# Kernel tuning notes

Hardware: AMD Instinct MI355X
Metric: run time of the kernel (lower is better)

## Reference

```python
import jax, jax.numpy as jnp
import numpy as np
import math

N_HEAD = 16

def _rope(x):
    # x: [B, H, T, D], D even; interleaved-pair rotation as in the torch code
    B, H, T, D = x.shape
    theta = 10000.0 ** (-2.0 * jnp.arange(D // 2, dtype=x.dtype) / D)  # [D/2]
    pos = jnp.arange(T, dtype=x.dtype)[:, None]                        # [T,1]
    ang = pos * theta[None, :]                                          # [T, D/2]
    sin, cos = jnp.sin(ang), jnp.cos(ang)
    x1, x2 = x[..., ::2], x[..., 1::2]
    x1r = x1 * cos - x2 * sin
    x2r = x1 * sin + x2 * cos
    # re-interleave
    out = jnp.stack([x1r, x2r], axis=-1).reshape(B, H, T, D)
    return out

def setup_inputs() -> dict:
    key = jax.random.key(0)
    ks = jax.random.split(key, 3)
    B, T, C = 4, 2048, 1024
    x = jax.random.normal(ks[0], (B, T, C), dtype=jnp.float32)
    W_qkv = jax.random.normal(ks[1], (C, 3 * C), dtype=jnp.float32) * (1.0 / math.sqrt(C))
    b_qkv = jnp.zeros((3 * C,), dtype=jnp.float32)
    W_proj = jax.random.normal(ks[2], (C, C), dtype=jnp.float32) * (1.0 / math.sqrt(C))
    b_proj = jnp.zeros((C,), dtype=jnp.float32)
    return {"x": x, "W_qkv": W_qkv, "b_qkv": b_qkv, "W_proj": W_proj, "b_proj": b_proj}

def reference(x, W_qkv, b_qkv, W_proj, b_proj):
    B, T, C = x.shape
    H = N_HEAD
    D = C // H
    qkv = x @ W_qkv + b_qkv                      # [B,T,3C]
    q, k, v = jnp.split(qkv, 3, axis=-1)
    def to_heads(t):
        return t.reshape(B, T, H, D).transpose(0, 2, 1, 3)  # [B,H,T,D]
    q, k, v = to_heads(q), to_heads(k), to_heads(v)
    q = _rope(q)
    k = _rope(k)
    att = jnp.einsum('bhqd,bhkd->bhqk', q, k) * (1.0 / math.sqrt(D))
    mask = jnp.tril(jnp.ones((T, T), dtype=bool))
    att = jnp.where(mask[None, None, :, :], att, -jnp.inf)
    att = jax.nn.softmax(att, axis=-1)
    y = jnp.einsum('bhqk,bhkd->bhqd', att, v)    # [B,H,T,D]
    y = y.transpose(0, 2, 1, 3).reshape(B, T, C)
    return y @ W_proj + b_proj
```

## Files before the change

### kernel.cpp

```cpp
#include <hip/hip_runtime.h>
#include <cstddef>

#define B_DIM 4
#define T_DIM 2048
#define C_DIM 1024
#define H_DIM 16
#define D_DIM 64
#define C3_DIM 3072

typedef __attribute__((ext_vector_type(8))) _Float16 f16x8;
typedef __attribute__((ext_vector_type(4))) _Float16 f16x4;
typedef __attribute__((ext_vector_type(4))) float f32x4;

typedef const __attribute__((address_space(1))) unsigned int* gptr_t;
typedef __attribute__((address_space(3))) unsigned int* lptr_t;

#define QSCALE 0.180336850073f
#define NTHETA 0.41524101186f

__global__ __launch_bounds__(256) void prep(
    const float* __restrict__ x, _Float16* __restrict__ xh,
    const float* __restrict__ Wq, _Float16* __restrict__ Wqt,
    const float* __restrict__ Wp, _Float16* __restrict__ Wpt)
{
    __shared__ float tile[64][65];
    const int z = blockIdx.x, tid = threadIdx.x;

    if (z < 8192) {
        size_t i = (size_t)z * 1024 + tid * 4;
        float4 v = *(const float4*)&x[i];
        f16x4 o = { (_Float16)v.x, (_Float16)v.y, (_Float16)v.z, (_Float16)v.w };
        *(f16x4*)&xh[i] = o;
        return;
    }

    const float* W;
    _Float16* Wt;
    int N, idx;
    if (z < 8960) { W = Wq; Wt = Wqt; N = C3_DIM; idx = z - 8192; }
    else          { W = Wp; Wt = Wpt; N = C_DIM;  idx = z - 8960; }
    const int K = C_DIM;
    const int nblk = N / 64;
    const int n0 = (idx % nblk) * 64, k0 = (idx / nblk) * 64;

    const int tx = tid & 15, ty = tid >> 4;
#pragma unroll
    for (int it = 0; it < 4; ++it) {
        int r = it * 16 + ty;
        *(float4*)&tile[r][tx * 4] =
            *(const float4*)&W[(size_t)(k0 + r) * N + n0 + tx * 4];
    }
    __syncthreads();
    int c = tid >> 2, t0 = (tid & 3) * 16;
    __align__(16) _Float16 tmp[16];
#pragma unroll
    for (int j = 0; j < 16; ++j) tmp[j] = (_Float16)tile[t0 + j][c];
    _Float16* o = Wt + (size_t)(n0 + c) * K + k0 + t0;
    *(f16x8*)o = *(f16x8*)&tmp[0];
    *(f16x8*)(o + 8) = *(f16x8*)&tmp[8];
}

#define ISSUE_SLICE(BUF, S, KT)                                               \
    do {                                                                      \
        const _Float16* agk = ag + (KT) * 64 + (S) * 32;                      \
        const _Float16* bgk = bg + (KT) * 64 + (S) * 32;                      \
        __builtin_amdgcn_global_load_lds((gptr_t)(const void*)(agk),          \
            (lptr_t)(void*)&Af[BUF][S][w * 2 + 0][0][0], 16, 0, 0);           \
        __builtin_amdgcn_global_load_lds((gptr_t)(const void*)(agk + 16 * K), \
            (lptr_t)(void*)&Af[BUF][S][w * 2 + 1][0][0], 16, 0, 0);           \
        __builtin_amdgcn_global_load_lds((gptr_t)(const void*)(bgk),          \
            (lptr_t)(void*)&Bf[BUF][S][w][0][0], 16, 0, 0);                   \
    } while (0)

#define COMPUTE_SLICE(BUF, S, SWAPPED)                                        \
    do {                                                                      \
        f16x8 av[4], bv[4];                                                   \
        _Pragma("unroll")                                                     \
        for (int i = 0; i < 4; ++i) {                                         \
            av[i] = *(const f16x8*)&Af[BUF][S][wm * 4 + i][lane][0];          \
            bv[i] = *(const f16x8*)&Bf[BUF][S][wn * 4 + i][lane][0];          \
        }                                                                     \
        __builtin_amdgcn_s_setprio(1);                                        \
        _Pragma("unroll")                                                     \
        for (int i = 0; i < 4; ++i)                                           \
            _Pragma("unroll")                                                 \
            for (int j = 0; j < 4; ++j)                                       \
                acc[i][j] = (SWAPPED)                                         \
                    ? __builtin_amdgcn_mfma_f32_16x16x32_f16(                 \
                          bv[j], av[i], acc[i][j], 0, 0, 0)                   \
                    : __builtin_amdgcn_mfma_f32_16x16x32_f16(                 \
                          av[i], bv[j], acc[i][j], 0, 0, 0);                  \
        __builtin_amdgcn_s_setprio(0);                                        \
    } while (0)

#define KLOOP(SWAPPED)                                                        \
    do {                                                                      \
        const int NT = K / 64;                                                \
        ISSUE_SLICE(0, 0, 0);                                                 \
        ISSUE_SLICE(0, 1, 0);                                                 \
        for (int t = 0; t < NT - 1; ++t) {                                    \
            const int cb = t & 1, nb = cb ^ 1;                                \
            ISSUE_SLICE(nb, 0, t + 1);                                        \
            asm volatile("s_waitcnt vmcnt(6)" ::: "memory");                  \
            __builtin_amdgcn_s_barrier();                                     \
            COMPUTE_SLICE(cb, 0, SWAPPED);                                    \
            ISSUE_SLICE(nb, 1, t + 1);                                        \
            asm volatile("s_waitcnt vmcnt(6)" ::: "memory");                  \
            __builtin_amdgcn_s_barrier();                                     \
            COMPUTE_SLICE(cb, 1, SWAPPED);                                    \
        }                                                                     \
        {                                                                     \
            const int cb = (NT - 1) & 1;                                      \
            asm volatile("s_waitcnt vmcnt(3)" ::: "memory");                  \
            __builtin_amdgcn_s_barrier();                                     \
            COMPUTE_SLICE(cb, 0, SWAPPED);                                    \
            asm volatile("s_waitcnt vmcnt(0)" ::: "memory");                  \
            __builtin_amdgcn_s_barrier();                                     \
            COMPUTE_SLICE(cb, 1, SWAPPED);                                    \
        }                                                                     \
    } while (0)

__global__ __launch_bounds__(512, 2) void gemm_qkv(
    const _Float16* __restrict__ A, const _Float16* __restrict__ Bt,
    const float* __restrict__ bias,
    _Float16* __restrict__ Qb, _Float16* __restrict__ Kb, _Float16* __restrict__ Vt)
{
    __shared__ __align__(16) _Float16 Af[2][2][16][64][8];
    __shared__ __align__(16) _Float16 Bf[2][2][8][64][8];
    const int tid = threadIdx.x;
    const int lane = tid & 63, w = tid >> 6;
    const int lm = lane & 15, lq = lane >> 4;
    const int wm = w >> 1, wn = w & 1;
    const int m0 = blockIdx.y * 256, n0 = blockIdx.x * 128;
    const int K = C_DIM;

    const _Float16* ag = A + (size_t)(m0 + w * 32 + lm) * K + lq * 8;
    const _Float16* bg = Bt + (size_t)(n0 + w * 16 + lm) * K + lq * 8;

    f32x4 acc[4][4];
#pragma unroll
    for (int i = 0; i < 4; ++i)
#pragma unroll
        for (int j = 0; j < 4; ++j) acc[i][j] = (f32x4){0.f, 0.f, 0.f, 0.f};

    const bool is_v = (n0 >= 2 * C_DIM);

    if (!is_v) {
        KLOOP(true);

        const bool is_q = (n0 < C_DIM);
        const float scale = is_q ? QSCALE : 1.0f;
        _Float16* dstbase = is_q ? Qb : Kb;
#pragma unroll
        for (int j = 0; j < 4; ++j) {
            int col = n0 + wn * 64 + j * 16 + lq * 4;
            int d0 = col & 63;
            int h = (col & (C_DIM - 1)) >> 6;
            float4 b4 = *(const float4*)&bias[col];
            float th0 = exp2f(-NTHETA * (float)(d0 >> 1));
            float th1 = exp2f(-NTHETA * (float)((d0 >> 1) + 1));
#pragma unroll
            for (int i = 0; i < 4; ++i) {
                int tg = m0 + wm * 64 + i * 16 + lm;
                int bb = tg >> 11, tl = tg & (T_DIM - 1);
                float v0 = acc[i][j][0] + b4.x;
                float v1 = acc[i][j][1] + b4.y;
                float v2 = acc[i][j][2] + b4.z;
                float v3 = acc[i][j][3] + b4.w;
                float s0, c0, s1, c1;
                __sincosf((float)tl * th0, &s0, &c0);
                __sincosf((float)tl * th1, &s1, &c1);
                f16x4 o = { (_Float16)((v0 * c0 - v1 * s0) * scale),
                            (_Float16)((v0 * s0 + v1 * c0) * scale),
                            (_Float16)((v2 * c1 - v3 * s1) * scale),
                            (_Float16)((v2 * s1 + v3 * c1) * scale) };
                *(f16x4*)&dstbase[((size_t)(bb * 16 + h) * T_DIM + tl) * 64 + d0] = o;
            }
        }
    } else {
        KLOOP(false);

#pragma unroll
        for (int i = 0; i < 4; ++i) {
            int t4 = m0 + wm * 64 + i * 16 + lq * 4;
            int bb = t4 >> 11, tl = t4 & (T_DIM - 1);
#pragma unroll
            for (int j = 0; j < 4; ++j) {
                int col = n0 + wn * 64 + j * 16 + lm;
                int dfull = col - 2 * C_DIM;
                int h = dfull >> 6, d = dfull & 63;
                float bc = bias[col];
                f16x4 o = { (_Float16)(acc[i][j][0] + bc),
                            (_Float16)(acc[i][j][1] + bc),
                            (_Float16)(acc[i][j][2] + bc),
                            (_Float16)(acc[i][j][3] + bc) };
                *(f16x4*)&Vt[((size_t)(bb * 16 + h) * 64 + d) * T_DIM + tl] = o;
            }
        }
    }
}

template <bool OUT_HALF>
__global__ __launch_bounds__(512, 2) void gemm_bt(
    const _Float16* __restrict__ A, const _Float16* __restrict__ Bt,
    const float* __restrict__ bias, void* __restrict__ Cout,
    int M, int N, int K)
{
    __shared__ __align__(16) _Float16 Af[2][2][16][64][8];
    __shared__ __align__(16) _Float16 Bf[2][2][8][64][8];
    const int tid = threadIdx.x;
    const int lane = tid & 63, w = tid >> 6;
    const int lm = lane & 15, lq = lane >> 4;
    const int wm = w >> 1, wn = w & 1;
    const int m0 = blockIdx.y * 256, n0 = blockIdx.x * 128;

    const _Float16* ag = A + (size_t)(m0 + w * 32 + lm) * K + lq * 8;
    const _Float16* bg = Bt + (size_t)(n0 + w * 16 + lm) * K + lq * 8;

    f32x4 acc[4][4];
#pragma unroll
    for (int i = 0; i < 4; ++i)
#pragma unroll
        for (int j = 0; j < 4; ++j) acc[i][j] = (f32x4){0.f, 0.f, 0.f, 0.f};

    KLOOP(true);

#pragma unroll
    for (int i = 0; i < 4; ++i) {
        size_t row = (size_t)(m0 + wm * 64 + i * 16 + lm);
#pragma unroll
        for (int j = 0; j < 4; ++j) {
            int col = n0 + wn * 64 + j * 16 + lq * 4;
            float4 b4 = *(const float4*)&bias[col];
            float v0 = acc[i][j][0] + b4.x;
            float v1 = acc[i][j][1] + b4.y;
            float v2 = acc[i][j][2] + b4.z;
            float v3 = acc[i][j][3] + b4.w;
            if (OUT_HALF) {
                f16x4 o = { (_Float16)v0, (_Float16)v1, (_Float16)v2, (_Float16)v3 };
                *(f16x4*)&((_Float16*)Cout)[row * N + col] = o;
            } else {
                float4 o = make_float4(v0, v1, v2, v3);
                *(float4*)&((float*)Cout)[row * N + col] = o;
            }
        }
    }
}

__global__ __launch_bounds__(256) void attn_mfma(
    const _Float16* __restrict__ Qb, const _Float16* __restrict__ Kb,
    const _Float16* __restrict__ Vt, _Float16* __restrict__ yb)
{
    __shared__ __align__(16) _Float16 Kf[8][64][8];
    __shared__ __align__(16) _Float16 Vf[8][64][8];
    __shared__ __align__(16) _Float16 Pb[4][16][72];

    const int tid = threadIdx.x;
    const int bh = blockIdx.x;
    const int qt = 31 - blockIdx.y;
    const int b = bh >> 4, h = bh & 15;
    const int lane = tid & 63, w = tid >> 6;
    const int m = lane & 15, qq = lane >> 4;

    const _Float16* qrow = Qb +
        ((size_t)bh * T_DIM + qt * 64 + w * 16 + m) * D_DIM + qq * 8;
    f16x8 qreg[2];
    qreg[0] = *(const f16x8*)qrow;
    qreg[1] = *(const f16x8*)(qrow + 32);

    float m_i = -1e30f, l_i = 0.f;
    f32x4 acc[4];
#pragma unroll
    for (int db = 0; db < 4; ++db) acc[db] = (f32x4){0.f, 0.f, 0.f, 0.f};

    const _Float16* kg0 = Kb + (size_t)bh * T_DIM * D_DIM +
                          (size_t)(w * 16 + m) * D_DIM + qq * 8;
    const _Float16* vg0 = Vt + (size_t)bh * D_DIM * T_DIM +
                          (size_t)(w * 16 + m) * T_DIM + qq * 8;

    f16x8 kr0 = *(const f16x8*)(kg0);
    f16x8 kr1 = *(const f16x8*)(kg0 + 32);
    f16x8 vr0 = *(const f16x8*)(vg0);
    f16x8 vr1 = *(const f16x8*)(vg0 + 32);

    for (int kt = 0; kt <= qt; ++kt) {
        __syncthreads();
        *(f16x8*)&Kf[w * 2 + 0][lane][0] = kr0;
        *(f16x8*)&Kf[w * 2 + 1][lane][0] = kr1;
        *(f16x8*)&Vf[w * 2 + 0][lane][0] = vr0;
        *(f16x8*)&Vf[w * 2 + 1][lane][0] = vr1;
        __syncthreads();

        int ktn = (kt < qt) ? kt + 1 : kt;
        kr0 = *(const f16x8*)(kg0 + (size_t)ktn * 64 * D_DIM);
        kr1 = *(const f16x8*)(kg0 + (size_t)ktn * 64 * D_DIM + 32);
        vr0 = *(const f16x8*)(vg0 + ktn * 64);
        vr1 = *(const f16x8*)(vg0 + ktn * 64 + 32);

        f32x4 sv[4];
#pragma unroll
        for (int nb = 0; nb < 4; ++nb) {
            f32x4 s = (f32x4){0.f, 0.f, 0.f, 0.f};
            s = __builtin_amdgcn_mfma_f32_16x16x32_f16(
                *(const f16x8*)&Kf[nb * 2 + 0][lane][0], qreg[0], s, 0, 0, 0);
            s = __builtin_amdgcn_mfma_f32_16x16x32_f16(
                *(const f16x8*)&Kf[nb * 2 + 1][lane][0], qreg[1], s, 0, 0, 0);
            sv[nb] = s;
        }

        if (kt == qt) {
            int qlocal = w * 16 + m;
#pragma unroll
            for (int nb = 0; nb < 4; ++nb) {
                int tb = nb * 16 + qq * 4;
#pragma unroll
                for (int r = 0; r < 4; ++r)
                    if (tb + r > qlocal) sv[nb][r] = -1e30f;
            }
        }

        float mt0 = fmaxf(fmaxf(sv[0][0], sv[0][1]), fmaxf(sv[0][2], sv[0][3]));
        float mt1 = fmaxf(fmaxf(sv[1][0], sv[1][1]), fmaxf(sv[1][2], sv[1][3]));
        float mt2 = fmaxf(fmaxf(sv[2][0], sv[2][1]), fmaxf(sv[2][2], sv[2][3]));
        float mt3 = fmaxf(fmaxf(sv[3][0], sv[3][1]), fmaxf(sv[3][2], sv[3][3]));
        float mt = fmaxf(fmaxf(mt0, mt1), fmaxf(mt2, mt3));
        mt = fmaxf(mt, __shfl_xor(mt, 16));
        mt = fmaxf(mt, __shfl_xor(mt, 32));
        float mnew = fmaxf(m_i, mt);
        float alpha = exp2f(m_i - mnew);
        float ll = 0.f;
#pragma unroll
        for (int nb = 0; nb < 4; ++nb) {
            float p0 = exp2f(sv[nb][0] - mnew);
            float p1 = exp2f(sv[nb][1] - mnew);
            float p2 = exp2f(sv[nb][2] - mnew);
            float p3 = exp2f(sv[nb][3] - mnew);
            sv[nb][0] = p0; sv[nb][1] = p1; sv[nb][2] = p2; sv[nb][3] = p3;
            ll += (p0 + p1) + (p2 + p3);
        }
        ll += __shfl_xor(ll, 16);
        ll += __shfl_xor(ll, 32);
        l_i = l_i * alpha + ll;
        m_i = mnew;
#pragma unroll
        for (int db = 0; db < 4; ++db) {
            acc[db][0] *= alpha; acc[db][1] *= alpha;
            acc[db][2] *= alpha; acc[db][3] *= alpha;
        }

#pragma unroll
        for (int nb = 0; nb < 4; ++nb) {
            f16x4 pv = { (_Float16)sv[nb][0], (_Float16)sv[nb][1],
                         (_Float16)sv[nb][2], (_Float16)sv[nb][3] };
            *(f16x4*)&Pb[w][m][nb * 16 + qq * 4] = pv;
        }

        f16x8 pf0 = *(const f16x8*)&Pb[w][m][0 * 32 + qq * 8];
        f16x8 pf1 = *(const f16x8*)&Pb[w][m][1 * 32 + qq * 8];

#pragma unroll
        for (int db = 0; db < 4; ++db) {
            acc[db] = __builtin_amdgcn_mfma_f32_16x16x32_f16(
                *(const f16x8*)&Vf[db * 2 + 0][lane][0], pf0, acc[db], 0, 0, 0);
            acc[db] = __builtin_amdgcn_mfma_f32_16x16x32_f16(
                *(const f16x8*)&Vf[db * 2 + 1][lane][0], pf1, acc[db], 0, 0, 0);
        }
    }

    float inv = 1.0f / l_i;
    _Float16* yrow = yb + (size_t)(b * T_DIM + qt * 64 + w * 16 + m) * C_DIM +
                     h * D_DIM + qq * 4;
#pragma unroll
    for (int db = 0; db < 4; ++db) {
        f16x4 o = { (_Float16)(acc[db][0] * inv), (_Float16)(acc[db][1] * inv),
                    (_Float16)(acc[db][2] * inv), (_Float16)(acc[db][3] * inv) };
        *(f16x4*)(yrow + db * 16) = o;
    }
}

extern "C" void kernel_launch(void* const* d_in, const int* in_sizes, int n_in,
                              void* d_out, int out_size, void* d_ws, size_t ws_size,
                              hipStream_t stream)
{
    const float* x     = (const float*)d_in[0];
    const float* Wqkv  = (const float*)d_in[1];
    const float* bqkv  = (const float*)d_in[2];
    const float* Wproj = (const float*)d_in[3];
    const float* bproj = (const float*)d_in[4];
    float* out = (float*)d_out;

    char* ws = (char*)d_ws;
    _Float16* xh  = (_Float16*)(ws);
    _Float16* yh  = (_Float16*)(ws + 16777216ull);
    _Float16* Qb  = (_Float16*)(ws + 33554432ull);
    _Float16* Kb  = (_Float16*)(ws + 50331648ull);
    _Float16* Vt  = (_Float16*)(ws + 67108864ull);
    _Float16* Wqt = (_Float16*)(ws + 83886080ull);
    _Float16* Wpt = (_Float16*)(ws + 90177536ull);

    prep<<<dim3(9216), dim3(256), 0, stream>>>(x, xh, Wqkv, Wqt, Wproj, Wpt);

    gemm_qkv<<<dim3(C3_DIM / 128, (B_DIM * T_DIM) / 256), dim3(512), 0, stream>>>(
        xh, Wqt, bqkv, Qb, Kb, Vt);

    attn_mfma<<<dim3(B_DIM * H_DIM, T_DIM / 64), dim3(256), 0, stream>>>(
        Qb, Kb, Vt, yh);

    gemm_bt<false><<<dim3(C_DIM / 128, (B_DIM * T_DIM) / 256), dim3(512), 0, stream>>>(
        yh, Wpt, bproj, out, B_DIM * T_DIM, C_DIM, C_DIM);
}
```

Measured before the change: 289.4 us.

## Switch GEMM k-loop to triple-buffered 32-wide slices and raise occupancy bound

The GEMM k-loop now cycles through a three-slot ring of 32-wide K slices, issuing the load two slices ahead, instead of double-buffered 64-wide tiles with two sub-slices each. This cuts LDS per block from 96 KB to 72 KB. Launch bounds are raised from 2 to 4 blocks per SM, which caps register usage at 64 VGPRs per thread. A 4x4 accumulator array (64 floats) cannot fit in that budget, so this risks spills, or the occupancy target is simply not met. The loop also now needs two barriers per 32-wide slice.

Result: slower. 307.5 us (+6.3%).

```diff
diff --git a/kernel.cpp b/kernel.cpp
--- a/kernel.cpp
+++ b/kernel.cpp
@@ -60,25 +60,25 @@
     *(f16x8*)(o + 8) = *(f16x8*)&tmp[8];
 }
 
-#define ISSUE_SLICE(BUF, S, KT)                                               \
+#define ISSUE_SLICE(BUF, S)                                                   \
     do {                                                                      \
-        const _Float16* agk = ag + (KT) * 64 + (S) * 32;                      \
-        const _Float16* bgk = bg + (KT) * 64 + (S) * 32;                      \
+        const _Float16* agk = ag + (S) * 32;                                  \
+        const _Float16* bgk = bg + (S) * 32;                                  \
         __builtin_amdgcn_global_load_lds((gptr_t)(const void*)(agk),          \
-            (lptr_t)(void*)&Af[BUF][S][w * 2 + 0][0][0], 16, 0, 0);           \
+            (lptr_t)(void*)&Af[BUF][w * 2 + 0][0][0], 16, 0, 0);              \
         __builtin_amdgcn_global_load_lds((gptr_t)(const void*)(agk + 16 * K), \
-            (lptr_t)(void*)&Af[BUF][S][w * 2 + 1][0][0], 16, 0, 0);           \
+            (lptr_t)(void*)&Af[BUF][w * 2 + 1][0][0], 16, 0, 0);              \
         __builtin_amdgcn_global_load_lds((gptr_t)(const void*)(bgk),          \
-            (lptr_t)(void*)&Bf[BUF][S][w][0][0], 16, 0, 0);                   \
+            (lptr_t)(void*)&Bf[BUF][w][0][0], 16, 0, 0);                      \
     } while (0)
 
-#define COMPUTE_SLICE(BUF, S, SWAPPED)                                        \
+#define COMPUTE_SLICE(BUF, SWAPPED)                                           \
     do {                                                                      \
         f16x8 av[4], bv[4];                                                   \
         _Pragma("unroll")                                                     \
         for (int i = 0; i < 4; ++i) {                                         \
-            av[i] = *(const f16x8*)&Af[BUF][S][wm * 4 + i][lane][0];          \
-            bv[i] = *(const f16x8*)&Bf[BUF][S][wn * 4 + i][lane][0];          \
+            av[i] = *(const f16x8*)&Af[BUF][wm * 4 + i][lane][0];             \
+            bv[i] = *(const f16x8*)&Bf[BUF][wn * 4 + i][lane][0];             \
         }                                                                     \
         __builtin_amdgcn_s_setprio(1);                                        \
         _Pragma("unroll")                                                     \
@@ -95,38 +95,34 @@
 
 #define KLOOP(SWAPPED)                                                        \
     do {                                                                      \
-        const int NT = K / 64;                                                \
-        ISSUE_SLICE(0, 0, 0);                                                 \
-        ISSUE_SLICE(0, 1, 0);                                                 \
-        for (int t = 0; t < NT - 1; ++t) {                                    \
-            const int cb = t & 1, nb = cb ^ 1;                                \
-            ISSUE_SLICE(nb, 0, t + 1);                                        \
-            asm volatile("s_waitcnt vmcnt(6)" ::: "memory");                  \
+        const int NS = K / 32;                                                \
+        ISSUE_SLICE(0, 0);                                                    \
+        ISSUE_SLICE(1, 1);                                                    \
+        int cur = 0;                                                          \
+        for (int s = 0; s < NS; ++s) {                                        \
+            if (s + 2 < NS) {                                                 \
+                int nb2 = cur + 2; if (nb2 >= 3) nb2 -= 3;                    \
+                ISSUE_SLICE(nb2, s + 2);                                      \
+                asm volatile("s_waitcnt vmcnt(6)" ::: "memory");              \
+            } else if (s + 2 == NS) {                                         \
+                asm volatile("s_waitcnt vmcnt(3)" ::: "memory");              \
+            } else {                                                          \
+                asm volatile("s_waitcnt vmcnt(0)" ::: "memory");              \
+            }                                                                 \
             __builtin_amdgcn_s_barrier();                                     \
-            COMPUTE_SLICE(cb, 0, SWAPPED);                                    \
-            ISSUE_SLICE(nb, 1, t + 1);                                        \
-            asm volatile("s_waitcnt vmcnt(6)" ::: "memory");                  \
-            __builtin_amdgcn_s_barrier();                                     \
-            COMPUTE_SLICE(cb, 1, SWAPPED);                                    \
-        }                                                                     \
-        {                                                                     \
-            const int cb = (NT - 1) & 1;                                      \
-            asm volatile("s_waitcnt vmcnt(3)" ::: "memory");                  \
-            __builtin_amdgcn_s_barrier();                                     \
-            COMPUTE_SLICE(cb, 0, SWAPPED);                                    \
-            asm volatile("s_waitcnt vmcnt(0)" ::: "memory");                  \
-            __builtin_amdgcn_s_barrier();                                     \
-            COMPUTE_SLICE(cb, 1, SWAPPED);                                    \
+            COMPUTE_SLICE(cur, SWAPPED);                                      \
+            if (s + 1 < NS) __builtin_amdgcn_s_barrier();                     \
+            ++cur; if (cur == 3) cur = 0;                                     \
         }                                                                     \
     } while (0)
 
-__global__ __launch_bounds__(512, 2) void gemm_qkv(
+__global__ __launch_bounds__(512, 4) void gemm_qkv(
     const _Float16* __restrict__ A, const _Float16* __restrict__ Bt,
     const float* __restrict__ bias,
     _Float16* __restrict__ Qb, _Float16* __restrict__ Kb, _Float16* __restrict__ Vt)
 {
-    __shared__ __align__(16) _Float16 Af[2][2][16][64][8];
-    __shared__ __align__(16) _Float16 Bf[2][2][8][64][8];
+    __shared__ __align__(16) _Float16 Af[3][16][64][8];
+    __shared__ __align__(16) _Float16 Bf[3][8][64][8];
     const int tid = threadIdx.x;
     const int lane = tid & 63, w = tid >> 6;
     const int lm = lane & 15, lq = lane >> 4;
@@ -201,13 +197,13 @@
 }
 
 template <bool OUT_HALF>
-__global__ __launch_bounds__(512, 2) void gemm_bt(
+__global__ __launch_bounds__(512, 4) void gemm_bt(
     const _Float16* __restrict__ A, const _Float16* __restrict__ Bt,
     const float* __restrict__ bias, void* __restrict__ Cout,
     int M, int N, int K)
 {
-    __shared__ __align__(16) _Float16 Af[2][2][16][64][8];
-    __shared__ __align__(16) _Float16 Bf[2][2][8][64][8];
+    __shared__ __align__(16) _Float16 Af[3][16][64][8];
+    __shared__ __align__(16) _Float16 Bf[3][8][64][8];
     const int tid = threadIdx.x;
     const int lane = tid & 63, w = tid >> 6;
     const int lm = lane & 15, lq = lane >> 4;
```

## Process two 64-row query tiles per attention block to reuse K/V tiles

Applied to the files above, without the earlier changes.

Each attention workgroup now handles 128 query rows as two 64-row halves, each with its own online-softmax state, and both halves share every K/V tile staged in shared memory. This roughly halves global K/V traffic and the number of barrier-synchronised staging steps per query row. In exchange the grid is halved to 1024 blocks, register use per thread doubles for Q and the accumulators, and block work becomes more uneven, which can lower occupancy and parallelism.

Result: no change. 294.0 us (+1.6%).

```diff
diff --git a/kernel.cpp b/kernel.cpp
--- a/kernel.cpp
+++ b/kernel.cpp
@@ -247,6 +247,73 @@
     }
 }
 
+#define ATTN_HALF(QREG, MI, LI, ACC, MASKKT)                                  \
+    do {                                                                      \
+        f32x4 sv[4];                                                          \
+        _Pragma("unroll")                                                     \
+        for (int nb = 0; nb < 4; ++nb) {                                      \
+            f32x4 s = (f32x4){0.f, 0.f, 0.f, 0.f};                            \
+            s = __builtin_amdgcn_mfma_f32_16x16x32_f16(                       \
+                *(const f16x8*)&Kf[nb * 2 + 0][lane][0], QREG[0], s, 0, 0, 0);\
+            s = __builtin_amdgcn_mfma_f32_16x16x32_f16(                       \
+                *(const f16x8*)&Kf[nb * 2 + 1][lane][0], QREG[1], s, 0, 0, 0);\
+            sv[nb] = s;                                                       \
+        }                                                                     \
+        if (kt == (MASKKT)) {                                                 \
+            int qlocal = w * 16 + m;                                          \
+            _Pragma("unroll")                                                 \
+            for (int nb = 0; nb < 4; ++nb) {                                  \
+                int tb = nb * 16 + qq * 4;                                    \
+                _Pragma("unroll")                                             \
+                for (int r = 0; r < 4; ++r)                                   \
+                    if (tb + r > qlocal) sv[nb][r] = -1e30f;                  \
+            }                                                                 \
+        }                                                                     \
+        float mt0 = fmaxf(fmaxf(sv[0][0], sv[0][1]), fmaxf(sv[0][2], sv[0][3]));\
+        float mt1 = fmaxf(fmaxf(sv[1][0], sv[1][1]), fmaxf(sv[1][2], sv[1][3]));\
+        float mt2 = fmaxf(fmaxf(sv[2][0], sv[2][1]), fmaxf(sv[2][2], sv[2][3]));\
+        float mt3 = fmaxf(fmaxf(sv[3][0], sv[3][1]), fmaxf(sv[3][2], sv[3][3]));\
+        float mt = fmaxf(fmaxf(mt0, mt1), fmaxf(mt2, mt3));                   \
+        mt = fmaxf(mt, __shfl_xor(mt, 16));                                   \
+        mt = fmaxf(mt, __shfl_xor(mt, 32));                                   \
+        float mnew = fmaxf(MI, mt);                                           \
+        float alpha = exp2f(MI - mnew);                                       \
+        float ll = 0.f;                                                       \
+        _Pragma("unroll")                                                     \
+        for (int nb = 0; nb < 4; ++nb) {                                      \
+            float p0 = exp2f(sv[nb][0] - mnew);                               \
+            float p1 = exp2f(sv[nb][1] - mnew);                               \
+            float p2 = exp2f(sv[nb][2] - mnew);                               \
+            float p3 = exp2f(sv[nb][3] - mnew);                               \
+            sv[nb][0] = p0; sv[nb][1] = p1; sv[nb][2] = p2; sv[nb][3] = p3;   \
+            ll += (p0 + p1) + (p2 + p3);                                      \
+        }                                                                     \
+        ll += __shfl_xor(ll, 16);                                             \
+        ll += __shfl_xor(ll, 32);                                             \
+        LI = LI * alpha + ll;                                                 \
+        MI = mnew;                                                            \
+        _Pragma("unroll")                                                     \
+        for (int db = 0; db < 4; ++db) {                                      \
+            ACC[db][0] *= alpha; ACC[db][1] *= alpha;                         \
+            ACC[db][2] *= alpha; ACC[db][3] *= alpha;                         \
+        }                                                                     \
+        _Pragma("unroll")                                                     \
+        for (int nb = 0; nb < 4; ++nb) {                                      \
+            f16x4 pv = { (_Float16)sv[nb][0], (_Float16)sv[nb][1],            \
+                         (_Float16)sv[nb][2], (_Float16)sv[nb][3] };          \
+            *(f16x4*)&Pb[w][m][nb * 16 + qq * 4] = pv;                        \
+        }                                                                     \
+        f16x8 pf0 = *(const f16x8*)&Pb[w][m][0 * 32 + qq * 8];                \
+        f16x8 pf1 = *(const f16x8*)&Pb[w][m][1 * 32 + qq * 8];                \
+        _Pragma("unroll")                                                     \
+        for (int db = 0; db < 4; ++db) {                                      \
+            ACC[db] = __builtin_amdgcn_mfma_f32_16x16x32_f16(                 \
+                *(const f16x8*)&Vf[db * 2 + 0][lane][0], pf0, ACC[db], 0, 0, 0);\
+            ACC[db] = __builtin_amdgcn_mfma_f32_16x16x32_f16(                 \
+                *(const f16x8*)&Vf[db * 2 + 1][lane][0], pf1, ACC[db], 0, 0, 0);\
+        }                                                                     \
+    } while (0)
+
 __global__ __launch_bounds__(256) void attn_mfma(
     const _Float16* __restrict__ Qb, const _Float16* __restrict__ Kb,
     const _Float16* __restrict__ Vt, _Float16* __restrict__ yb)
@@ -257,21 +324,28 @@
 
     const int tid = threadIdx.x;
     const int bh = blockIdx.x;
-    const int qt = 31 - blockIdx.y;
+    const int qt = 15 - blockIdx.y;
+    const int qt2 = 2 * qt;
+    const int ktmax = 2 * qt + 1;
     const int b = bh >> 4, h = bh & 15;
     const int lane = tid & 63, w = tid >> 6;
     const int m = lane & 15, qq = lane >> 4;
 
-    const _Float16* qrow = Qb +
-        ((size_t)bh * T_DIM + qt * 64 + w * 16 + m) * D_DIM + qq * 8;
-    f16x8 qreg[2];
-    qreg[0] = *(const f16x8*)qrow;
-    qreg[1] = *(const f16x8*)(qrow + 32);
-
-    float m_i = -1e30f, l_i = 0.f;
-    f32x4 acc[4];
-#pragma unroll
-    for (int db = 0; db < 4; ++db) acc[db] = (f32x4){0.f, 0.f, 0.f, 0.f};
+    const _Float16* qrowA = Qb +
+        ((size_t)bh * T_DIM + qt * 128 + w * 16 + m) * D_DIM + qq * 8;
+    f16x8 qregA[2], qregB[2];
+    qregA[0] = *(const f16x8*)qrowA;
+    qregA[1] = *(const f16x8*)(qrowA + 32);
+    qregB[0] = *(const f16x8*)(qrowA + 64 * D_DIM);
+    qregB[1] = *(const f16x8*)(qrowA + 64 * D_DIM + 32);
+
+    float mA = -1e30f, lA = 0.f, mB = -1e30f, lB = 0.f;
+    f32x4 accA[4], accB[4];
+#pragma unroll
+    for (int db = 0; db < 4; ++db) {
+        accA[db] = (f32x4){0.f, 0.f, 0.f, 0.f};
+        accB[db] = (f32x4){0.f, 0.f, 0.f, 0.f};
+    }
 
     const _Float16* kg0 = Kb + (size_t)bh * T_DIM * D_DIM +
                           (size_t)(w * 16 + m) * D_DIM + qq * 8;
@@ -283,7 +357,7 @@
     f16x8 vr0 = *(const f16x8*)(vg0);
     f16x8 vr1 = *(const f16x8*)(vg0 + 32);
 
-    for (int kt = 0; kt <= qt; ++kt) {
+    for (int kt = 0; kt <= ktmax; ++kt) {
         __syncthreads();
         *(f16x8*)&Kf[w * 2 + 0][lane][0] = kr0;
         *(f16x8*)&Kf[w * 2 + 1][lane][0] = kr1;
@@ -291,90 +365,39 @@
         *(f16x8*)&Vf[w * 2 + 1][lane][0] = vr1;
         __syncthreads();
 
-        int ktn = (kt < qt) ? kt + 1 : kt;
+        int ktn = (kt < ktmax) ? kt + 1 : kt;
         kr0 = *(const f16x8*)(kg0 + (size_t)ktn * 64 * D_DIM);
         kr1 = *(const f16x8*)(kg0 + (size_t)ktn * 64 * D_DIM + 32);
         vr0 = *(const f16x8*)(vg0 + ktn * 64);
         vr1 = *(const f16x8*)(vg0 + ktn * 64 + 32);
 
-        f32x4 sv[4];
-#pragma unroll
-        for (int nb = 0; nb < 4; ++nb) {
-            f32x4 s = (f32x4){0.f, 0.f, 0.f, 0.f};
-            s = __builtin_amdgcn_mfma_f32_16x16x32_f16(
-                *(const f16x8*)&Kf[nb * 2 + 0][lane][0], qreg[0], s, 0, 0, 0);
-            s = __builtin_amdgcn_mfma_f32_16x16x32_f16(
-                *(const f16x8*)&Kf[nb * 2 + 1][lane][0], qreg[1], s, 0, 0, 0);
-            sv[nb] = s;
+        if (kt <= qt2) { ATTN_HALF(qregA, mA, lA, accA, qt2); }
+        { ATTN_HALF(qregB, mB, lB, accB, ktmax); }
+    }
+
+    {
+        float inv = 1.0f / lA;
+        _Float16* yrow = yb +
+            (size_t)(b * T_DIM + qt * 128 + w * 16 + m) * C_DIM +
+            h * D_DIM + qq * 4;
+#pragma unroll
+        for (int db = 0; db < 4; ++db) {
+            f16x4 o = { (_Float16)(accA[db][0] * inv), (_Float16)(accA[db][1] * inv),
+                        (_Float16)(accA[db][2] * inv), (_Float16)(accA[db][3] * inv) };
+            *(f16x4*)(yrow + db * 16) = o;
         }
-
-        if (kt == qt) {
-            int qlocal = w * 16 + m;
-#pragma unroll
-            for (int nb = 0; nb < 4; ++nb) {
-                int tb = nb * 16 + qq * 4;
-#pragma unroll
-                for (int r = 0; r < 4; ++r)
-                    if (tb + r > qlocal) sv[nb][r] = -1e30f;
-            }
+    }
+    {
+        float inv = 1.0f / lB;
+        _Float16* yrow = yb +
+            (size_t)(b * T_DIM + qt * 128 + 64 + w * 16 + m) * C_DIM +
+            h * D_DIM + qq * 4;
+#pragma unroll
+        for (int db = 0; db < 4; ++db) {
+            f16x4 o = { (_Float16)(accB[db][0] * inv), (_Float16)(accB[db][1] * inv),
+                        (_Float16)(accB[db][2] * inv), (_Float16)(accB[db][3] * inv) };
+            *(f16x4*)(yrow + db * 16) = o;
         }
-
-        float mt0 = fmaxf(fmaxf(sv[0][0], sv[0][1]), fmaxf(sv[0][2], sv[0][3]));
-        float mt1 = fmaxf(fmaxf(sv[1][0], sv[1][1]), fmaxf(sv[1][2], sv[1][3]));
-        float mt2 = fmaxf(fmaxf(sv[2][0], sv[2][1]), fmaxf(sv[2][2], sv[2][3]));
-        float mt3 = fmaxf(fmaxf(sv[3][0], sv[3][1]), fmaxf(sv[3][2], sv[3][3]));
-        float mt = fmaxf(fmaxf(mt0, mt1), fmaxf(mt2, mt3));
-        mt = fmaxf(mt, __shfl_xor(mt, 16));
-        mt = fmaxf(mt, __shfl_xor(mt, 32));
-        float mnew = fmaxf(m_i, mt);
-        float alpha = exp2f(m_i - mnew);
-        float ll = 0.f;
-#pragma unroll
-        for (int nb = 0; nb < 4; ++nb) {
-            float p0 = exp2f(sv[nb][0] - mnew);
-            float p1 = exp2f(sv[nb][1] - mnew);
-            float p2 = exp2f(sv[nb][2] - mnew);
-            float p3 = exp2f(sv[nb][3] - mnew);
-            sv[nb][0] = p0; sv[nb][1] = p1; sv[nb][2] = p2; sv[nb][3] = p3;
-            ll += (p0 + p1) + (p2 + p3);
-        }
-        ll += __shfl_xor(ll, 16);
-        ll += __shfl_xor(ll, 32);
-        l_i = l_i * alpha + ll;
-        m_i = mnew;
-#pragma unroll
-        for (int db = 0; db < 4; ++db) {
-            acc[db][0] *= alpha; acc[db][1] *= alpha;
-            acc[db][2] *= alpha; acc[db][3] *= alpha;
-        }
-
-#pragma unroll
-        for (int nb = 0; nb < 4; ++nb) {
-            f16x4 pv = { (_Float16)sv[nb][0], (_Float16)sv[nb][1],
-                         (_Float16)sv[nb][2], (_Float16)sv[nb][3] };
-            *(f16x4*)&Pb[w][m][nb * 16 + qq * 4] = pv;
-        }
-
-        f16x8 pf0 = *(const f16x8*)&Pb[w][m][0 * 32 + qq * 8];
-        f16x8 pf1 = *(const f16x8*)&Pb[w][m][1 * 32 + qq * 8];
-
-#pragma unroll
-        for (int db = 0; db < 4; ++db) {
-            acc[db] = __builtin_amdgcn_mfma_f32_16x16x32_f16(
-                *(const f16x8*)&Vf[db * 2 + 0][lane][0], pf0, acc[db], 0, 0, 0);
-            acc[db] = __builtin_amdgcn_mfma_f32_16x16x32_f16(
-                *(const f16x8*)&Vf[db * 2 + 1][lane][0], pf1, acc[db], 0, 0, 0);
-        }
-    }
-
-    float inv = 1.0f / l_i;
-    _Float16* yrow = yb + (size_t)(b * T_DIM + qt * 64 + w * 16 + m) * C_DIM +
-                     h * D_DIM + qq * 4;
-#pragma unroll
-    for (int db = 0; db < 4; ++db) {
-        f16x4 o = { (_Float16)(acc[db][0] * inv), (_Float16)(acc[db][1] * inv),
-                    (_Float16)(acc[db][2] * inv), (_Float16)(acc[db][3] * inv) };
-        *(f16x4*)(yrow + db * 16) = o;
     }
 }
 
@@ -403,7 +426,7 @@
     gemm_qkv<<<dim3(C3_DIM / 128, (B_DIM * T_DIM) / 256), dim3(512), 0, stream>>>(
         xh, Wqt, bqkv, Qb, Kb, Vt);
 
-    attn_mfma<<<dim3(B_DIM * H_DIM, T_DIM / 64), dim3(256), 0, stream>>>(
+    attn_mfma<<<dim3(B_DIM * H_DIM, T_DIM / 128), dim3(256), 0, stream>>>(
         Qb, Kb, Vt, yh);
 
     gemm_bt<false><<<dim3(C_DIM / 128, (B_DIM * T_DIM) / 256), dim3(512), 0, stream>>>(
```
